# Performance work log

Measured on AMD Instinct MI355X. Metric: run time of the kernel, lower is better.

The kernel has to match this reference:

```python
import jax, jax.numpy as jnp
import numpy as np

B, T, C = 16, 2048, 1024
HEAD = 64

def setup_inputs() -> dict:
    key = jax.random.key(0)
    kx, kq, kk, kv = jax.random.split(key, 4)
    x = jax.random.normal(kx, (B, T, C), dtype=jnp.float32)
    s = 1.0 / np.sqrt(C)
    Wq = jax.random.normal(kq, (C, HEAD), dtype=jnp.float32) * s
    Wk = jax.random.normal(kk, (C, HEAD), dtype=jnp.float32) * s
    Wv = jax.random.normal(kv, (C, HEAD), dtype=jnp.float32) * s
    return {"x": x, "Wq": Wq, "Wk": Wk, "Wv": Wv}

def reference(x, Wq, Wk, Wv):
    Bb, Tt, Cc = x.shape
    q = jnp.einsum('btc,ch->bth', x, Wq)  # [B,T,H]
    k = jnp.einsum('btc,ch->bth', x, Wk)
    v = jnp.einsum('btc,ch->bth', x, Wv)
    # NOTE: source scales by C**-0.5 (n_embd), not head_size**-0.5
    scores = jnp.einsum('bth,bsh->bts', q, k) * (Cc ** -0.5)  # [B,T,T]
    causal = jnp.tril(jnp.ones((Tt, Tt), dtype=bool))
    scores = jnp.where(causal, scores, -jnp.inf)
    attn = jax.nn.softmax(scores, axis=-1)  # dropout p=0 -> identity
    out = jnp.einsum('bts,bsh->bth', attn, v)  # [B,T,H]
    return out
```

## Files before the change

### kernel.cpp

```cpp
#include <hip/hip_runtime.h>

typedef __bf16 bf16;
typedef __bf16 bf16x2 __attribute__((ext_vector_type(2)));
typedef __bf16 bf16x4 __attribute__((ext_vector_type(4)));
typedef __bf16 bf16x8 __attribute__((ext_vector_type(8)));
typedef float f32x4 __attribute__((ext_vector_type(4)));

#define TT_ 2048
#define CC_ 1024
#define HH_ 64

#define SCALE2 0.045084221f

static __device__ __forceinline__ unsigned pack_bf16(float a, float b) {
    union { bf16x2 h; unsigned u; } z;
    z.h = bf16x2{(bf16)a, (bf16)b};
    return z.u;
}
static __device__ __forceinline__ void plswap32(unsigned &a, unsigned &b) {
    asm("v_permlane32_swap_b32 %0, %1" : "+v"(a), "+v"(b));
}
static __device__ __forceinline__ void plswap16(unsigned &a, unsigned &b) {
    asm("v_permlane16_swap_b32 %0, %1" : "+v"(a), "+v"(b));
}

__global__ __launch_bounds__(256) void prep_w(const float* __restrict__ Wq,
                                              const float* __restrict__ Wk,
                                              const float* __restrict__ Wv,
                                              bf16* __restrict__ Wt) {
    __shared__ bf16 Ls[64 * 65];
    const int m  = blockIdx.x >> 4;
    const int k0 = (blockIdx.x & 15) * 64;
    const float* W = (m == 0) ? Wq : (m == 1) ? Wk : Wv;
    const int tid = threadIdx.x;
    #pragma unroll
    for (int j = 0; j < 4; ++j) {
        int idx = tid + 256 * j;
        int r   = idx >> 4;
        int c4  = (idx & 15) * 4;
        float4 w = *(const float4*)&W[(size_t)(k0 + r) * HH_ + c4];
        Ls[r * 65 + c4 + 0] = (bf16)w.x;
        Ls[r * 65 + c4 + 1] = (bf16)w.y;
        Ls[r * 65 + c4 + 2] = (bf16)w.z;
        Ls[r * 65 + c4 + 3] = (bf16)w.w;
    }
    __syncthreads();
    #pragma unroll
    for (int j = 0; j < 4; ++j) {
        int idx = tid + 256 * j;
        int n   = idx >> 4;
        int kc  = (idx & 15) * 4;
        bf16x4 v;
        #pragma unroll
        for (int i = 0; i < 4; ++i) v[i] = Ls[(kc + i) * 65 + n];
        *(bf16x4*)&Wt[m * 65536 + n * 1024 + k0 + kc] = v;
    }
}

#define QKV_STEP(KBI, BU, BP, XLD, XWR)                                        \
    {                                                                          \
        const int k0 = (KBI) * 64;                                             \
        __syncthreads();                                                       \
        if ((KBI) < 14) {                                                      \
            _Pragma("unroll")                                                  \
            for (int rr = 0; rr < 4; ++rr)                                     \
                XLD[rr] = *(const float4*)&x[(size_t)(m0 + srow + rr * 16) * CC_ + k0 + 128 + scol]; \
        }                                                                      \
        if ((KBI) < 15) {                                                      \
            _Pragma("unroll")                                                  \
            for (int step = 0; step < 2; ++step)                               \
                _Pragma("unroll")                                              \
                for (int ct = 0; ct < 3; ++ct)                                 \
                    BP[step][ct] = *(const bf16x8*)&Wt[(size_t)(wave * 48 + ct * 16 + lane) * 1024 + k0 + 64 + step * 32 + quad * 8]; \
        }                                                                      \
        bf16x8 afr[2][4];                                                      \
        _Pragma("unroll")                                                      \
        for (int step = 0; step < 2; ++step)                                   \
            _Pragma("unroll")                                                  \
            for (int rt = 0; rt < 4; ++rt)                                     \
                afr[step][rt] = *(const bf16x8*)&Xs[(KBI) & 1][(rt * 16 + lane) * 72 + step * 32 + quad * 8]; \
        _Pragma("unroll")                                                      \
        for (int step = 0; step < 2; ++step)                                   \
            _Pragma("unroll")                                                  \
            for (int ct = 0; ct < 3; ++ct)                                     \
                _Pragma("unroll")                                              \
                for (int rt = 0; rt < 4; ++rt)                                 \
                    acc[rt][ct] = __builtin_amdgcn_mfma_f32_16x16x32_bf16(afr[step][rt], BU[step][ct], acc[rt][ct], 0, 0, 0); \
        if ((KBI) < 15) {                                                      \
            _Pragma("unroll")                                                  \
            for (int rr = 0; rr < 4; ++rr) {                                   \
                bf16x4 bv = {(bf16)XWR[rr].x, (bf16)XWR[rr].y, (bf16)XWR[rr].z, (bf16)XWR[rr].w}; \
                *(bf16x4*)&Xs[((KBI) + 1) & 1][(srow + rr * 16) * 72 + scol] = bv; \
            }                                                                  \
        }                                                                      \
    }

__global__ __launch_bounds__(256, 2) void qkv_kernel(const float* __restrict__ x,
                                                     const bf16* __restrict__ Wt,
                                                     bf16* __restrict__ qb,
                                                     bf16* __restrict__ kb,
                                                     bf16* __restrict__ vt) {
    __shared__ __align__(16) bf16 Xs[2][64 * 72];
    const int tid  = threadIdx.x;
    const int wave = tid >> 6;
    const int lane = tid & 15;
    const int quad = (tid & 63) >> 4;
    const int m0   = blockIdx.x * 64;

    f32x4 acc[4][3];
    #pragma unroll
    for (int i = 0; i < 4; ++i)
        #pragma unroll
        for (int j = 0; j < 3; ++j) acc[i][j] = f32x4{0.f, 0.f, 0.f, 0.f};

    const int srow = tid >> 4;
    const int scol = (tid & 15) * 4;

    {
        float4 x0[4];
        #pragma unroll
        for (int rr = 0; rr < 4; ++rr)
            x0[rr] = *(const float4*)&x[(size_t)(m0 + srow + rr * 16) * CC_ + scol];
        #pragma unroll
        for (int rr = 0; rr < 4; ++rr) {
            bf16x4 bv = {(bf16)x0[rr].x, (bf16)x0[rr].y, (bf16)x0[rr].z, (bf16)x0[rr].w};
            *(bf16x4*)&Xs[0][(srow + rr * 16) * 72 + scol] = bv;
        }
    }
    float4 xS0[4], xS1[4];
    #pragma unroll
    for (int rr = 0; rr < 4; ++rr)
        xS1[rr] = *(const float4*)&x[(size_t)(m0 + srow + rr * 16) * CC_ + 64 + scol];
    bf16x8 bfrA[2][3], bfrB[2][3];
    #pragma unroll
    for (int step = 0; step < 2; ++step)
        #pragma unroll
        for (int ct = 0; ct < 3; ++ct)
            bfrA[step][ct] = *(const bf16x8*)&Wt[(size_t)(wave * 48 + ct * 16 + lane) * 1024 + step * 32 + quad * 8];

    for (int kb2 = 0; kb2 < 16; kb2 += 2) {
        QKV_STEP(kb2,     bfrA, bfrB, xS0, xS1)
        QKV_STEP(kb2 + 1, bfrB, bfrA, xS1, xS0)
    }

    const int bb = m0 >> 11;
    const int t0 = m0 & 2047;
    __syncthreads();
    #pragma unroll
    for (int ct = 0; ct < 3; ++ct) {
        int c0 = wave * 48 + ct * 16;
        if (c0 < 64) {
            int h = c0 + lane;
            #pragma unroll
            for (int rt = 0; rt < 4; ++rt)
                #pragma unroll
                for (int r = 0; r < 4; ++r)
                    qb[(size_t)(m0 + rt * 16 + quad * 4 + r) * HH_ + h] = (bf16)(acc[rt][ct][r] * SCALE2);
        } else if (c0 < 128) {
            int h = (c0 - 64) + lane;
            #pragma unroll
            for (int rt = 0; rt < 4; ++rt)
                #pragma unroll
                for (int r = 0; r < 4; ++r)
                    kb[(size_t)(m0 + rt * 16 + quad * 4 + r) * HH_ + h] = (bf16)acc[rt][ct][r];
        } else {
            int h = (c0 - 128) + lane;
            #pragma unroll
            for (int rt = 0; rt < 4; ++rt)
                #pragma unroll
                for (int r = 0; r < 4; ++r)
                    Xs[0][(rt * 16 + quad * 4 + r) * 72 + h] = (bf16)acc[rt][ct][r];
        }
    }
    __syncthreads();
    {
        int h  = tid >> 2;
        int tc = (tid & 3) * 16;
        bf16x8 v0, v1;
        #pragma unroll
        for (int i = 0; i < 8; ++i) v0[i] = Xs[0][(tc + i) * 72 + h];
        #pragma unroll
        for (int i = 0; i < 8; ++i) v1[i] = Xs[0][(tc + 8 + i) * 72 + h];
        bf16* dst = &vt[(size_t)bb * HH_ * TT_ + (size_t)h * TT_ + t0 + tc];
        *(bf16x8*)dst = v0;
        *(bf16x8*)(dst + 8) = v1;
    }
}

__global__ __launch_bounds__(256, 2) void attn_kernel(const bf16* __restrict__ qb,
                                                      const bf16* __restrict__ kb,
                                                      const bf16* __restrict__ vt,
                                                      float* __restrict__ out) {
    __shared__ __align__(16) bf16 Ks[128 * 72];
    __shared__ __align__(16) bf16 Vs[64 * 136];

    const int tid  = threadIdx.x;
    const int wave = tid >> 6;
    const int lane = tid & 15;
    const int quad = (tid & 63) >> 4;

    const int j  = blockIdx.x;
    const int bb = j & 15;
    const int p  = j >> 4;
    const int qi = (p < 16) ? p : 47 - p;
    const int nch = (qi >> 1) + 1;

    const int qrow  = qi * 64 + wave * 16;
    const int qg    = qrow + lane;
    const int qmaxw = qrow + 15;

    const int krow = tid >> 3, kc8 = (tid & 7) * 8;
    const int vh   = tid >> 4, vc8 = (tid & 15) * 8;
    const bf16* kp = kb + (size_t)(bb * TT_ + krow) * HH_ + kc8;
    const bf16* vp = vt + (size_t)bb * HH_ * TT_ + (size_t)vh * TT_ + vc8;

    bf16x8 kr[4], vvr[4];
    #pragma unroll
    for (int j2 = 0; j2 < 4; ++j2) kr[j2]  = *(const bf16x8*)&kp[(size_t)j2 * 32 * HH_];
    #pragma unroll
    for (int j2 = 0; j2 < 4; ++j2) vvr[j2] = *(const bf16x8*)&vp[j2 * 16 * TT_];

    bf16x8 aq[2];
    #pragma unroll
    for (int step = 0; step < 2; ++step)
        aq[step] = *(const bf16x8*)&qb[(size_t)(bb * TT_ + qg) * HH_ + step * 32 + quad * 8];

    bf16x8 vones;
    #pragma unroll
    for (int i = 0; i < 8; ++i) vones[i] = (bf16)1.0f;

    f32x4 o_acc[4];
    #pragma unroll
    for (int ht = 0; ht < 4; ++ht) o_acc[ht] = f32x4{0.f, 0.f, 0.f, 0.f};
    f32x4 lacc = f32x4{0.f, 0.f, 0.f, 0.f};

    for (int c = 0; c < nch; ++c) {
        const int s0 = c * 128;
        __syncthreads();
        #pragma unroll
        for (int j2 = 0; j2 < 4; ++j2) *(bf16x8*)&Ks[(krow + 32 * j2) * 72 + kc8] = kr[j2];
        #pragma unroll
        for (int j2 = 0; j2 < 4; ++j2) *(bf16x8*)&Vs[(vh + 16 * j2) * 136 + vc8]  = vvr[j2];
        __syncthreads();
        if (c + 1 < nch) {
            #pragma unroll
            for (int j2 = 0; j2 < 4; ++j2)
                kr[j2] = *(const bf16x8*)&kp[(size_t)((c + 1) * 128 + j2 * 32) * HH_];
            #pragma unroll
            for (int j2 = 0; j2 < 4; ++j2)
                vvr[j2] = *(const bf16x8*)&vp[(c + 1) * 128 + j2 * 16 * TT_];
        }

        const bool msk = (c == nch - 1);
        #pragma unroll
        for (int w = 0; w < 4; ++w) {
            if (msk && (s0 + w * 32 > qmaxw)) continue;
            const bool haveB = !msk || (s0 + w * 32 + 16 <= qmaxw);

            f32x4 sA = {0.f, 0.f, 0.f, 0.f};
            f32x4 sB = {0.f, 0.f, 0.f, 0.f};
            __builtin_amdgcn_s_setprio(1);
            {
                bf16x8 ak0 = *(const bf16x8*)&Ks[(w * 32 + lane) * 72 + quad * 8];
                bf16x8 ak1 = *(const bf16x8*)&Ks[(w * 32 + lane) * 72 + 32 + quad * 8];
                sA = __builtin_amdgcn_mfma_f32_16x16x32_bf16(ak0, aq[0], sA, 0, 0, 0);
                sA = __builtin_amdgcn_mfma_f32_16x16x32_bf16(ak1, aq[1], sA, 0, 0, 0);
            }
            if (haveB) {
                bf16x8 bk0 = *(const bf16x8*)&Ks[(w * 32 + 16 + lane) * 72 + quad * 8];
                bf16x8 bk1 = *(const bf16x8*)&Ks[(w * 32 + 16 + lane) * 72 + 32 + quad * 8];
                sB = __builtin_amdgcn_mfma_f32_16x16x32_bf16(bk0, aq[0], sB, 0, 0, 0);
                sB = __builtin_amdgcn_mfma_f32_16x16x32_bf16(bk1, aq[1], sB, 0, 0, 0);
            }
            __builtin_amdgcn_s_setprio(0);

            const int kA0 = s0 + w * 32 + quad * 4;
            float eA[4], eB[4];
            #pragma unroll
            for (int r = 0; r < 4; ++r) {
                float e = __builtin_amdgcn_exp2f(sA[r]);
                if (msk && (kA0 + r > qg)) e = 0.f;
                eA[r] = e;
            }
            if (haveB) {
                #pragma unroll
                for (int r = 0; r < 4; ++r) {
                    float e = __builtin_amdgcn_exp2f(sB[r]);
                    if (msk && (kA0 + 16 + r > qg)) e = 0.f;
                    eB[r] = e;
                }
            } else {
                #pragma unroll
                for (int r = 0; r < 4; ++r) eB[r] = 0.f;
            }

            unsigned d0 = pack_bf16(eA[0], eA[1]);
            unsigned d1 = pack_bf16(eA[2], eA[3]);
            unsigned d2 = pack_bf16(eB[0], eB[1]);
            unsigned d3 = pack_bf16(eB[2], eB[3]);
            plswap32(d0, d2);
            plswap16(d0, d2);
            plswap32(d1, d3);
            plswap16(d1, d3);
            union { unsigned u[4]; bf16x8 v; } apu;
            apu.u[0] = d0; apu.u[1] = d1; apu.u[2] = d2; apu.u[3] = d3;

            __builtin_amdgcn_s_setprio(1);
            #pragma unroll
            for (int ht = 0; ht < 4; ++ht) {
                bf16x8 bv = *(const bf16x8*)&Vs[(ht * 16 + lane) * 136 + w * 32 + quad * 8];
                o_acc[ht] = __builtin_amdgcn_mfma_f32_16x16x32_bf16(apu.v, bv, o_acc[ht], 0, 0, 0);
            }
            lacc = __builtin_amdgcn_mfma_f32_16x16x32_bf16(apu.v, vones, lacc, 0, 0, 0);
            __builtin_amdgcn_s_setprio(0);
        }
    }

    float inv[4];
    #pragma unroll
    for (int r = 0; r < 4; ++r) inv[r] = __builtin_amdgcn_rcpf(lacc[r]);
    #pragma unroll
    for (int ht = 0; ht < 4; ++ht)
        #pragma unroll
        for (int r = 0; r < 4; ++r)
            out[(size_t)(bb * TT_ + qrow + quad * 4 + r) * HH_ + ht * 16 + lane] = o_acc[ht][r] * inv[r];
}

extern "C" void kernel_launch(void* const* d_in, const int* in_sizes, int n_in,
                              void* d_out, int out_size, void* d_ws, size_t ws_size,
                              hipStream_t stream) {
    const float* x  = (const float*)d_in[0];
    const float* Wq = (const float*)d_in[1];
    const float* Wk = (const float*)d_in[2];
    const float* Wv = (const float*)d_in[3];
    float* out = (float*)d_out;

    char* ws = (char*)d_ws;
    bf16*  qb = (bf16*)(ws);
    bf16*  kb = (bf16*)(ws + 4194304);
    bf16*  vt = (bf16*)(ws + 8388608);
    bf16*  Wt = (bf16*)(ws + 12582912);

    prep_w<<<48, 256, 0, stream>>>(Wq, Wk, Wv, Wt);
    qkv_kernel<<<512, 256, 0, stream>>>(x, Wt, qb, kb, vt);
    attn_kernel<<<512, 256, 0, stream>>>(qb, kb, vt, out);
}
```

Baseline: 238.1 us.

## Halve QKV tile rows and split attention key blocks across two wave groups

The QKV projection now uses 32-row tiles across 1024 blocks with occupancy 4, and drops the register double-buffering of weight fragments in favour of a simpler loop. The attention kernel doubles its block to 512 threads, with two wave groups each handling half of the 32-key sub-blocks for the same query rows. Their partial outputs and row sums are combined through shared memory at the end. The aim is more parallelism and occupancy, at the cost of an extra reduction and sync and less latency hiding in the QKV loads.

```diff
diff --git a/kernel.cpp b/kernel.cpp
--- a/kernel.cpp
+++ b/kernel.cpp
@@ -57,90 +57,67 @@
     }
 }
 
-#define QKV_STEP(KBI, BU, BP, XLD, XWR)                                        \
-    {                                                                          \
-        const int k0 = (KBI) * 64;                                             \
-        __syncthreads();                                                       \
-        if ((KBI) < 14) {                                                      \
-            _Pragma("unroll")                                                  \
-            for (int rr = 0; rr < 4; ++rr)                                     \
-                XLD[rr] = *(const float4*)&x[(size_t)(m0 + srow + rr * 16) * CC_ + k0 + 128 + scol]; \
-        }                                                                      \
-        if ((KBI) < 15) {                                                      \
-            _Pragma("unroll")                                                  \
-            for (int step = 0; step < 2; ++step)                               \
-                _Pragma("unroll")                                              \
-                for (int ct = 0; ct < 3; ++ct)                                 \
-                    BP[step][ct] = *(const bf16x8*)&Wt[(size_t)(wave * 48 + ct * 16 + lane) * 1024 + k0 + 64 + step * 32 + quad * 8]; \
-        }                                                                      \
-        bf16x8 afr[2][4];                                                      \
-        _Pragma("unroll")                                                      \
-        for (int step = 0; step < 2; ++step)                                   \
-            _Pragma("unroll")                                                  \
-            for (int rt = 0; rt < 4; ++rt)                                     \
-                afr[step][rt] = *(const bf16x8*)&Xs[(KBI) & 1][(rt * 16 + lane) * 72 + step * 32 + quad * 8]; \
-        _Pragma("unroll")                                                      \
-        for (int step = 0; step < 2; ++step)                                   \
-            _Pragma("unroll")                                                  \
-            for (int ct = 0; ct < 3; ++ct)                                     \
-                _Pragma("unroll")                                              \
-                for (int rt = 0; rt < 4; ++rt)                                 \
-                    acc[rt][ct] = __builtin_amdgcn_mfma_f32_16x16x32_bf16(afr[step][rt], BU[step][ct], acc[rt][ct], 0, 0, 0); \
-        if ((KBI) < 15) {                                                      \
-            _Pragma("unroll")                                                  \
-            for (int rr = 0; rr < 4; ++rr) {                                   \
-                bf16x4 bv = {(bf16)XWR[rr].x, (bf16)XWR[rr].y, (bf16)XWR[rr].z, (bf16)XWR[rr].w}; \
-                *(bf16x4*)&Xs[((KBI) + 1) & 1][(srow + rr * 16) * 72 + scol] = bv; \
-            }                                                                  \
-        }                                                                      \
-    }
-
-__global__ __launch_bounds__(256, 2) void qkv_kernel(const float* __restrict__ x,
+__global__ __launch_bounds__(256, 4) void qkv_kernel(const float* __restrict__ x,
                                                      const bf16* __restrict__ Wt,
                                                      bf16* __restrict__ qb,
                                                      bf16* __restrict__ kb,
                                                      bf16* __restrict__ vt) {
-    __shared__ __align__(16) bf16 Xs[2][64 * 72];
+    __shared__ __align__(16) bf16 Xs[2][32 * 72];
     const int tid  = threadIdx.x;
     const int wave = tid >> 6;
     const int lane = tid & 15;
     const int quad = (tid & 63) >> 4;
-    const int m0   = blockIdx.x * 64;
-
-    f32x4 acc[4][3];
-    #pragma unroll
-    for (int i = 0; i < 4; ++i)
+    const int m0   = blockIdx.x * 32;
+
+    f32x4 acc[2][3];
+    #pragma unroll
+    for (int i = 0; i < 2; ++i)
         #pragma unroll
         for (int j = 0; j < 3; ++j) acc[i][j] = f32x4{0.f, 0.f, 0.f, 0.f};
 
-    const int srow = tid >> 4;
-    const int scol = (tid & 15) * 4;
-
+    const int srow = tid >> 3;
+    const int sc8  = (tid & 7) * 8;
+
+    float4 xr0 = *(const float4*)&x[(size_t)(m0 + srow) * CC_ + sc8];
+    float4 xr1 = *(const float4*)&x[(size_t)(m0 + srow) * CC_ + sc8 + 4];
     {
-        float4 x0[4];
-        #pragma unroll
-        for (int rr = 0; rr < 4; ++rr)
-            x0[rr] = *(const float4*)&x[(size_t)(m0 + srow + rr * 16) * CC_ + scol];
-        #pragma unroll
-        for (int rr = 0; rr < 4; ++rr) {
-            bf16x4 bv = {(bf16)x0[rr].x, (bf16)x0[rr].y, (bf16)x0[rr].z, (bf16)x0[rr].w};
-            *(bf16x4*)&Xs[0][(srow + rr * 16) * 72 + scol] = bv;
-        }
-    }
-    float4 xS0[4], xS1[4];
-    #pragma unroll
-    for (int rr = 0; rr < 4; ++rr)
-        xS1[rr] = *(const float4*)&x[(size_t)(m0 + srow + rr * 16) * CC_ + 64 + scol];
-    bf16x8 bfrA[2][3], bfrB[2][3];
-    #pragma unroll
-    for (int step = 0; step < 2; ++step)
-        #pragma unroll
-        for (int ct = 0; ct < 3; ++ct)
-            bfrA[step][ct] = *(const bf16x8*)&Wt[(size_t)(wave * 48 + ct * 16 + lane) * 1024 + step * 32 + quad * 8];
-
-    for (int kb2 = 0; kb2 < 16; kb2 += 2) {
-        QKV_STEP(kb2,     bfrA, bfrB, xS0, xS1)
-        QKV_STEP(kb2 + 1, bfrB, bfrA, xS1, xS0)
+        bf16x8 bv = {(bf16)xr0.x, (bf16)xr0.y, (bf16)xr0.z, (bf16)xr0.w,
+                     (bf16)xr1.x, (bf16)xr1.y, (bf16)xr1.z, (bf16)xr1.w};
+        *(bf16x8*)&Xs[0][srow * 72 + sc8] = bv;
+    }
+
+    for (int kbi = 0; kbi < 16; ++kbi) {
+        const int cur = kbi & 1;
+        const int k0  = kbi * 64;
+        __syncthreads();
+        if (kbi < 15) {
+            xr0 = *(const float4*)&x[(size_t)(m0 + srow) * CC_ + k0 + 64 + sc8];
+            xr1 = *(const float4*)&x[(size_t)(m0 + srow) * CC_ + k0 + 64 + sc8 + 4];
+        }
+        bf16x8 bfr[2][3];
+        #pragma unroll
+        for (int step = 0; step < 2; ++step)
+            #pragma unroll
+            for (int ct = 0; ct < 3; ++ct)
+                bfr[step][ct] = *(const bf16x8*)&Wt[(size_t)(wave * 48 + ct * 16 + lane) * 1024 + k0 + step * 32 + quad * 8];
+        bf16x8 afr[2][2];
+        #pragma unroll
+        for (int step = 0; step < 2; ++step)
+            #pragma unroll
+            for (int rt = 0; rt < 2; ++rt)
+                afr[step][rt] = *(const bf16x8*)&Xs[cur][(rt * 16 + lane) * 72 + step * 32 + quad * 8];
+        #pragma unroll
+        for (int step = 0; step < 2; ++step)
+            #pragma unroll
+            for (int ct = 0; ct < 3; ++ct)
+                #pragma unroll
+                for (int rt = 0; rt < 2; ++rt)
+                    acc[rt][ct] = __builtin_amdgcn_mfma_f32_16x16x32_bf16(afr[step][rt], bfr[step][ct], acc[rt][ct], 0, 0, 0);
+        if (kbi < 15) {
+            bf16x8 bv = {(bf16)xr0.x, (bf16)xr0.y, (bf16)xr0.z, (bf16)xr0.w,
+                         (bf16)xr1.x, (bf16)xr1.y, (bf16)xr1.z, (bf16)xr1.w};
+            *(bf16x8*)&Xs[cur ^ 1][srow * 72 + sc8] = bv;
+        }
     }
 
     const int bb = m0 >> 11;
@@ -152,21 +129,21 @@
         if (c0 < 64) {
             int h = c0 + lane;
             #pragma unroll
-            for (int rt = 0; rt < 4; ++rt)
+            for (int rt = 0; rt < 2; ++rt)
                 #pragma unroll
                 for (int r = 0; r < 4; ++r)
                     qb[(size_t)(m0 + rt * 16 + quad * 4 + r) * HH_ + h] = (bf16)(acc[rt][ct][r] * SCALE2);
         } else if (c0 < 128) {
             int h = (c0 - 64) + lane;
             #pragma unroll
-            for (int rt = 0; rt < 4; ++rt)
+            for (int rt = 0; rt < 2; ++rt)
                 #pragma unroll
                 for (int r = 0; r < 4; ++r)
                     kb[(size_t)(m0 + rt * 16 + quad * 4 + r) * HH_ + h] = (bf16)acc[rt][ct][r];
         } else {
             int h = (c0 - 128) + lane;
             #pragma unroll
-            for (int rt = 0; rt < 4; ++rt)
+            for (int rt = 0; rt < 2; ++rt)
                 #pragma unroll
                 for (int r = 0; r < 4; ++r)
                     Xs[0][(rt * 16 + quad * 4 + r) * 72 + h] = (bf16)acc[rt][ct][r];
@@ -175,19 +152,15 @@
     __syncthreads();
     {
         int h  = tid >> 2;
-        int tc = (tid & 3) * 16;
-        bf16x8 v0, v1;
+        int tc = (tid & 3) * 8;
+        bf16x8 v0;
         #pragma unroll
         for (int i = 0; i < 8; ++i) v0[i] = Xs[0][(tc + i) * 72 + h];
-        #pragma unroll
-        for (int i = 0; i < 8; ++i) v1[i] = Xs[0][(tc + 8 + i) * 72 + h];
-        bf16* dst = &vt[(size_t)bb * HH_ * TT_ + (size_t)h * TT_ + t0 + tc];
-        *(bf16x8*)dst = v0;
-        *(bf16x8*)(dst + 8) = v1;
-    }
-}
-
-__global__ __launch_bounds__(256, 2) void attn_kernel(const bf16* __restrict__ qb,
+        *(bf16x8*)&vt[(size_t)bb * HH_ * TT_ + (size_t)h * TT_ + t0 + tc] = v0;
+    }
+}
+
+__global__ __launch_bounds__(512, 4) void attn_kernel(const bf16* __restrict__ qb,
                                                       const bf16* __restrict__ kb,
                                                       const bf16* __restrict__ vt,
                                                       float* __restrict__ out) {
@@ -196,16 +169,18 @@
 
     const int tid  = threadIdx.x;
     const int wave = tid >> 6;
+    const int qw   = wave & 3;
+    const int kg   = wave >> 2;
     const int lane = tid & 15;
     const int quad = (tid & 63) >> 4;
 
-    const int j  = blockIdx.x;
-    const int bb = j & 15;
-    const int p  = j >> 4;
+    const int jb = blockIdx.x;
+    const int bb = jb & 15;
+    const int p  = jb >> 4;
     const int qi = (p < 16) ? p : 47 - p;
     const int nch = (qi >> 1) + 1;
 
-    const int qrow  = qi * 64 + wave * 16;
+    const int qrow  = qi * 64 + qw * 16;
     const int qg    = qrow + lane;
     const int qmaxw = qrow + 15;
 
@@ -214,11 +189,11 @@
     const bf16* kp = kb + (size_t)(bb * TT_ + krow) * HH_ + kc8;
     const bf16* vp = vt + (size_t)bb * HH_ * TT_ + (size_t)vh * TT_ + vc8;
 
-    bf16x8 kr[4], vvr[4];
-    #pragma unroll
-    for (int j2 = 0; j2 < 4; ++j2) kr[j2]  = *(const bf16x8*)&kp[(size_t)j2 * 32 * HH_];
-    #pragma unroll
-    for (int j2 = 0; j2 < 4; ++j2) vvr[j2] = *(const bf16x8*)&vp[j2 * 16 * TT_];
+    bf16x8 kr[2], vvr[2];
+    #pragma unroll
+    for (int jj = 0; jj < 2; ++jj) kr[jj]  = *(const bf16x8*)&kp[(size_t)jj * 64 * HH_];
+    #pragma unroll
+    for (int jj = 0; jj < 2; ++jj) vvr[jj] = *(const bf16x8*)&vp[jj * 32 * TT_];
 
     bf16x8 aq[2];
     #pragma unroll
@@ -238,22 +213,23 @@
         const int s0 = c * 128;
         __syncthreads();
         #pragma unroll
-        for (int j2 = 0; j2 < 4; ++j2) *(bf16x8*)&Ks[(krow + 32 * j2) * 72 + kc8] = kr[j2];
-        #pragma unroll
-        for (int j2 = 0; j2 < 4; ++j2) *(bf16x8*)&Vs[(vh + 16 * j2) * 136 + vc8]  = vvr[j2];
+        for (int jj = 0; jj < 2; ++jj) *(bf16x8*)&Ks[(krow + 64 * jj) * 72 + kc8] = kr[jj];
+        #pragma unroll
+        for (int jj = 0; jj < 2; ++jj) *(bf16x8*)&Vs[(vh + 32 * jj) * 136 + vc8]  = vvr[jj];
         __syncthreads();
         if (c + 1 < nch) {
             #pragma unroll
-            for (int j2 = 0; j2 < 4; ++j2)
-                kr[j2] = *(const bf16x8*)&kp[(size_t)((c + 1) * 128 + j2 * 32) * HH_];
-            #pragma unroll
-            for (int j2 = 0; j2 < 4; ++j2)
-                vvr[j2] = *(const bf16x8*)&vp[(c + 1) * 128 + j2 * 16 * TT_];
+            for (int jj = 0; jj < 2; ++jj)
+                kr[jj] = *(const bf16x8*)&kp[(size_t)((c + 1) * 128 + jj * 64) * HH_];
+            #pragma unroll
+            for (int jj = 0; jj < 2; ++jj)
+                vvr[jj] = *(const bf16x8*)&vp[(c + 1) * 128 + jj * 32 * TT_];
         }
 
         const bool msk = (c == nch - 1);
         #pragma unroll
-        for (int w = 0; w < 4; ++w) {
+        for (int wi = 0; wi < 2; ++wi) {
+            const int w = kg + wi * 2;
             if (msk && (s0 + w * 32 > qmaxw)) continue;
             const bool haveB = !msk || (s0 + w * 32 + 16 <= qmaxw);
 
@@ -316,14 +292,37 @@
         }
     }
 
-    float inv[4];
-    #pragma unroll
-    for (int r = 0; r < 4; ++r) inv[r] = __builtin_amdgcn_rcpf(lacc[r]);
-    #pragma unroll
-    for (int ht = 0; ht < 4; ++ht)
+    __syncthreads();
+    float* cbuf = (float*)Ks;
+    float* lbuf = cbuf + 64 * 65;
+    if (kg == 1) {
+        #pragma unroll
+        for (int ht = 0; ht < 4; ++ht)
+            #pragma unroll
+            for (int r = 0; r < 4; ++r)
+                cbuf[(qw * 16 + quad * 4 + r) * 65 + ht * 16 + lane] = o_acc[ht][r];
+        if (lane == 0) {
+            #pragma unroll
+            for (int r = 0; r < 4; ++r) lbuf[qw * 16 + quad * 4 + r] = lacc[r];
+        }
+    }
+    __syncthreads();
+    if (kg == 0) {
+        #pragma unroll
+        for (int ht = 0; ht < 4; ++ht)
+            #pragma unroll
+            for (int r = 0; r < 4; ++r)
+                o_acc[ht][r] += cbuf[(qw * 16 + quad * 4 + r) * 65 + ht * 16 + lane];
+        float inv[4];
         #pragma unroll
         for (int r = 0; r < 4; ++r)
-            out[(size_t)(bb * TT_ + qrow + quad * 4 + r) * HH_ + ht * 16 + lane] = o_acc[ht][r] * inv[r];
+            inv[r] = __builtin_amdgcn_rcpf(lacc[r] + lbuf[qw * 16 + quad * 4 + r]);
+        #pragma unroll
+        for (int ht = 0; ht < 4; ++ht)
+            #pragma unroll
+            for (int r = 0; r < 4; ++r)
+                out[(size_t)(bb * TT_ + qrow + quad * 4 + r) * HH_ + ht * 16 + lane] = o_acc[ht][r] * inv[r];
+    }
 }
 
 extern "C" void kernel_launch(void* const* d_in, const int* in_sizes, int n_in,
@@ -342,6 +341,6 @@
     bf16*  Wt = (bf16*)(ws + 12582912);
 
     prep_w<<<48, 256, 0, stream>>>(Wq, Wk, Wv, Wt);
-    qkv_kernel<<<512, 256, 0, stream>>>(x, Wt, qb, kb, vt);
-    attn_kernel<<<512, 256, 0, stream>>>(qb, kb, vt, out);
-}
+    qkv_kernel<<<1024, 256, 0, stream>>>(x, Wt, qb, kb, vt);
+    attn_kernel<<<512, 512, 0, stream>>>(qb, kb, vt, out);
+}
```

Measured after the change: 249.3 us. 1.05x slower.

## Load QKV projection operands directly from global memory, dropping LDS double buffering

Applied to the files above, without the earlier changes.

The QKV projection kernel no longer stages x tiles through double-buffered shared memory with register prefetch. Each wave now reads its MFMA A-fragments straight from global fp32 x and converts them to bf16 in registers, and B-fragments are loaded per iteration without prefetch. Launch bounds are raised to 3 blocks per CU. This removes the LDS traffic and barriers, but every one of the 4 waves now reloads the same x rows, so global and L2 traffic on x goes up roughly fourfold. The explicit software pipelining that hid load latency is also gone.

```diff
diff --git a/kernel.cpp b/kernel.cpp
--- a/kernel.cpp
+++ b/kernel.cpp
@@ -57,50 +57,12 @@
     }
 }
 
-#define QKV_STEP(KBI, BU, BP, XLD, XWR)                                        \
-    {                                                                          \
-        const int k0 = (KBI) * 64;                                             \
-        __syncthreads();                                                       \
-        if ((KBI) < 14) {                                                      \
-            _Pragma("unroll")                                                  \
-            for (int rr = 0; rr < 4; ++rr)                                     \
-                XLD[rr] = *(const float4*)&x[(size_t)(m0 + srow + rr * 16) * CC_ + k0 + 128 + scol]; \
-        }                                                                      \
-        if ((KBI) < 15) {                                                      \
-            _Pragma("unroll")                                                  \
-            for (int step = 0; step < 2; ++step)                               \
-                _Pragma("unroll")                                              \
-                for (int ct = 0; ct < 3; ++ct)                                 \
-                    BP[step][ct] = *(const bf16x8*)&Wt[(size_t)(wave * 48 + ct * 16 + lane) * 1024 + k0 + 64 + step * 32 + quad * 8]; \
-        }                                                                      \
-        bf16x8 afr[2][4];                                                      \
-        _Pragma("unroll")                                                      \
-        for (int step = 0; step < 2; ++step)                                   \
-            _Pragma("unroll")                                                  \
-            for (int rt = 0; rt < 4; ++rt)                                     \
-                afr[step][rt] = *(const bf16x8*)&Xs[(KBI) & 1][(rt * 16 + lane) * 72 + step * 32 + quad * 8]; \
-        _Pragma("unroll")                                                      \
-        for (int step = 0; step < 2; ++step)                                   \
-            _Pragma("unroll")                                                  \
-            for (int ct = 0; ct < 3; ++ct)                                     \
-                _Pragma("unroll")                                              \
-                for (int rt = 0; rt < 4; ++rt)                                 \
-                    acc[rt][ct] = __builtin_amdgcn_mfma_f32_16x16x32_bf16(afr[step][rt], BU[step][ct], acc[rt][ct], 0, 0, 0); \
-        if ((KBI) < 15) {                                                      \
-            _Pragma("unroll")                                                  \
-            for (int rr = 0; rr < 4; ++rr) {                                   \
-                bf16x4 bv = {(bf16)XWR[rr].x, (bf16)XWR[rr].y, (bf16)XWR[rr].z, (bf16)XWR[rr].w}; \
-                *(bf16x4*)&Xs[((KBI) + 1) & 1][(srow + rr * 16) * 72 + scol] = bv; \
-            }                                                                  \
-        }                                                                      \
-    }
-
-__global__ __launch_bounds__(256, 2) void qkv_kernel(const float* __restrict__ x,
+__global__ __launch_bounds__(256, 3) void qkv_kernel(const float* __restrict__ x,
                                                      const bf16* __restrict__ Wt,
                                                      bf16* __restrict__ qb,
                                                      bf16* __restrict__ kb,
                                                      bf16* __restrict__ vt) {
-    __shared__ __align__(16) bf16 Xs[2][64 * 72];
+    __shared__ __align__(16) bf16 Xs[64 * 72];
     const int tid  = threadIdx.x;
     const int wave = tid >> 6;
     const int lane = tid & 15;
@@ -113,39 +75,41 @@
         #pragma unroll
         for (int j = 0; j < 3; ++j) acc[i][j] = f32x4{0.f, 0.f, 0.f, 0.f};
 
-    const int srow = tid >> 4;
-    const int scol = (tid & 15) * 4;
-
-    {
-        float4 x0[4];
-        #pragma unroll
-        for (int rr = 0; rr < 4; ++rr)
-            x0[rr] = *(const float4*)&x[(size_t)(m0 + srow + rr * 16) * CC_ + scol];
-        #pragma unroll
-        for (int rr = 0; rr < 4; ++rr) {
-            bf16x4 bv = {(bf16)x0[rr].x, (bf16)x0[rr].y, (bf16)x0[rr].z, (bf16)x0[rr].w};
-            *(bf16x4*)&Xs[0][(srow + rr * 16) * 72 + scol] = bv;
-        }
-    }
-    float4 xS0[4], xS1[4];
-    #pragma unroll
-    for (int rr = 0; rr < 4; ++rr)
-        xS1[rr] = *(const float4*)&x[(size_t)(m0 + srow + rr * 16) * CC_ + 64 + scol];
-    bf16x8 bfrA[2][3], bfrB[2][3];
-    #pragma unroll
-    for (int step = 0; step < 2; ++step)
-        #pragma unroll
-        for (int ct = 0; ct < 3; ++ct)
-            bfrA[step][ct] = *(const bf16x8*)&Wt[(size_t)(wave * 48 + ct * 16 + lane) * 1024 + step * 32 + quad * 8];
-
-    for (int kb2 = 0; kb2 < 16; kb2 += 2) {
-        QKV_STEP(kb2,     bfrA, bfrB, xS0, xS1)
-        QKV_STEP(kb2 + 1, bfrB, bfrA, xS1, xS0)
+    const float* xrow[4];
+    #pragma unroll
+    for (int rt = 0; rt < 4; ++rt)
+        xrow[rt] = x + (size_t)(m0 + rt * 16 + lane) * CC_ + quad * 8;
+    const bf16* wbase = Wt + (size_t)(wave * 48 + lane) * 1024 + quad * 8;
+
+    for (int kbi = 0; kbi < 16; ++kbi) {
+        const int k0 = kbi * 64;
+        bf16x8 afr[2][4];
+        #pragma unroll
+        for (int step = 0; step < 2; ++step)
+            #pragma unroll
+            for (int rt = 0; rt < 4; ++rt) {
+                float4 a = *(const float4*)&xrow[rt][k0 + step * 32];
+                float4 b = *(const float4*)&xrow[rt][k0 + step * 32 + 4];
+                afr[step][rt] = bf16x8{(bf16)a.x, (bf16)a.y, (bf16)a.z, (bf16)a.w,
+                                       (bf16)b.x, (bf16)b.y, (bf16)b.z, (bf16)b.w};
+            }
+        bf16x8 bfr[2][3];
+        #pragma unroll
+        for (int step = 0; step < 2; ++step)
+            #pragma unroll
+            for (int ct = 0; ct < 3; ++ct)
+                bfr[step][ct] = *(const bf16x8*)&wbase[(size_t)(ct * 16) * 1024 + k0 + step * 32];
+        #pragma unroll
+        for (int step = 0; step < 2; ++step)
+            #pragma unroll
+            for (int ct = 0; ct < 3; ++ct)
+                #pragma unroll
+                for (int rt = 0; rt < 4; ++rt)
+                    acc[rt][ct] = __builtin_amdgcn_mfma_f32_16x16x32_bf16(afr[step][rt], bfr[step][ct], acc[rt][ct], 0, 0, 0);
     }
 
     const int bb = m0 >> 11;
     const int t0 = m0 & 2047;
-    __syncthreads();
     #pragma unroll
     for (int ct = 0; ct < 3; ++ct) {
         int c0 = wave * 48 + ct * 16;
@@ -169,7 +133,7 @@
             for (int rt = 0; rt < 4; ++rt)
                 #pragma unroll
                 for (int r = 0; r < 4; ++r)
-                    Xs[0][(rt * 16 + quad * 4 + r) * 72 + h] = (bf16)acc[rt][ct][r];
+                    Xs[(rt * 16 + quad * 4 + r) * 72 + h] = (bf16)acc[rt][ct][r];
         }
     }
     __syncthreads();
@@ -178,9 +142,9 @@
         int tc = (tid & 3) * 16;
         bf16x8 v0, v1;
         #pragma unroll
-        for (int i = 0; i < 8; ++i) v0[i] = Xs[0][(tc + i) * 72 + h];
-        #pragma unroll
-        for (int i = 0; i < 8; ++i) v1[i] = Xs[0][(tc + 8 + i) * 72 + h];
+        for (int i = 0; i < 8; ++i) v0[i] = Xs[(tc + i) * 72 + h];
+        #pragma unroll
+        for (int i = 0; i < 8; ++i) v1[i] = Xs[(tc + 8 + i) * 72 + h];
         bf16* dst = &vt[(size_t)bb * HH_ * TT_ + (size_t)h * TT_ + t0 + tc];
         *(bf16x8*)dst = v0;
         *(bf16x8*)(dst + 8) = v1;
```

Result: slower. 289.2 us (+21.5%).
